# Kernel tuning notes

Measured on AMD Instinct MI355X. Metric: run time of the kernel, lower is better.

## Reference

```python
import jax, jax.numpy as jnp
import numpy as np
from jax import lax

T, B, S = 64, 32, 64
V, E, H = 32000, 512, 512

def _p(key, shape, scale=0.05):
    return (jax.random.normal(key, shape, dtype=jnp.float32) * scale)

def setup_inputs() -> dict:
    key = jax.random.key(0)
    ks = jax.random.split(key, 24)
    inp = {
        'trg': jax.random.randint(ks[0], (T, B), 0, V),
        'encoded_src': jax.random.normal(ks[1], (S, B, 2 * H), dtype=jnp.float32),
        'emb': _p(ks[2], (V, E)),
        # LSTM layer 0: input = E + 2H
        'W_ih0': _p(ks[3], (4 * H, E + 2 * H)), 'W_hh0': _p(ks[4], (4 * H, H)),
        'b_ih0': _p(ks[5], (4 * H,)), 'b_hh0': _p(ks[6], (4 * H,)),
        # LSTM layer 1: input = H
        'W_ih1': _p(ks[7], (4 * H, H)), 'W_hh1': _p(ks[8], (4 * H, H)),
        'b_ih1': _p(ks[9], (4 * H,)), 'b_hh1': _p(ks[10], (4 * H,)),
        # attn_annot: 2H -> H
        'Wa': _p(ks[11], (H, 2 * H)), 'ba': _p(ks[12], (H,)),
        # attn_hidden: H -> H
        'Wh': _p(ks[13], (H, H)), 'bh': _p(ks[14], (H,)),
        # other: H -> 1
        'Wo': _p(ks[15], (1, H)), 'bo': _p(ks[16], (1,)),
        # penult: 3H -> E
        'Wp': _p(ks[17], (E, 3 * H)), 'bp': _p(ks[18], (E,)),
        # out bias (weight tied to emb)
        'b_out': _p(ks[19], (V,)),
    }
    return inp

def _lstm_cell(x, h, c, W_ih, W_hh, b_ih, b_hh):
    # PyTorch gate order: i, f, g, o
    g = x @ W_ih.T + b_ih + h @ W_hh.T + b_hh
    i, f, gg, o = jnp.split(g, 4, axis=-1)
    c_new = jax.nn.sigmoid(f) * c + jax.nn.sigmoid(i) * jnp.tanh(gg)
    h_new = jax.nn.sigmoid(o) * jnp.tanh(c_new)
    return h_new, c_new

def reference(trg, encoded_src, emb, W_ih0, W_hh0, b_ih0, b_hh0,
              W_ih1, W_hh1, b_ih1, b_hh1, Wa, ba, Wh, bh, Wo, bo,
              Wp, bp, b_out):
    trg_emb = emb[trg]                                # [T,B,E]
    annot_scores = encoded_src @ Wa.T + ba            # [S,B,H]
    Hd = W_hh0.shape[1]
    Bd = encoded_src.shape[1]
    h0 = jnp.zeros((2, Bd, Hd), dtype=encoded_src.dtype)
    c0 = jnp.zeros((2, Bd, Hd), dtype=encoded_src.dtype)
    ctx0 = jnp.zeros((Bd, encoded_src.shape[2]), dtype=encoded_src.dtype)

    def step(carry, emb_t):
        h, c, ctx = carry
        x = jnp.concatenate([emb_t, ctx], axis=1)      # [B, E+2H]
        h0n, c0n = _lstm_cell(x,   h[0], c[0], W_ih0, W_hh0, b_ih0, b_hh0)
        h1n, c1n = _lstm_cell(h0n, h[1], c[1], W_ih1, W_hh1, b_ih1, b_hh1)
        out = h1n                                      # [B,H]
        hs = out @ Wh.T + bh                           # [B,H]
        e = jnp.tanh(hs[None] + annot_scores) @ Wo.T + bo   # [S,B,1]
        a = jax.nn.softmax(e, axis=0)[..., 0]          # [S,B]
        ctx_new = jnp.einsum('sb,sbd->bd', a, encoded_src)  # [B,2H]
        stacked = jnp.concatenate([out, ctx_new], axis=1)   # [B,3H]
        return (jnp.stack([h0n, h1n]), jnp.stack([c0n, c1n]), ctx_new), stacked

    (h, c, _), all_scores = lax.scan(step, (h0, c0, ctx0), trg_emb)  # all_scores [T,B,3H]
    pen = all_scores @ Wp.T + bp                       # [T,B,E]
    logits = pen @ emb.T + b_out                       # [T,B,V] (tied weights)
    scores = jax.nn.log_softmax(logits, axis=2)
    return (scores, h, c)
```

## Files before the change

### kernel.cpp

```cpp
#include <hip/hip_runtime.h>


typedef unsigned short u16;
typedef short bf16x8 __attribute__((ext_vector_type(8)));
typedef float f32x4 __attribute__((ext_vector_type(4)));

#define MFMA_BF16(a, b, c) __builtin_amdgcn_mfma_f32_16x16x32_bf16((a), (b), (c), 0, 0, 0)

struct __attribute__((aligned(8))) U16x4 { u16 x, y, z, w; };

__device__ __forceinline__ float b2f(u16 u) {
  unsigned v = ((unsigned)u) << 16; float f; __builtin_memcpy(&f, &v, 4); return f;
}
__device__ __forceinline__ u16 f2b(float f) {
  unsigned u; __builtin_memcpy(&u, &f, 4);
  u = (u + 0x7FFFu + ((u >> 16) & 1u)) >> 16;
  return (u16)u;
}
__device__ __forceinline__ float sigm(float x) { return 1.f / (1.f + __expf(-x)); }
__device__ __forceinline__ float tanh_fast(float x) {
  x = fminf(fmaxf(x, -15.f), 15.f);
  float e = __expf(2.f * x);
  return (e - 1.f) / (e + 1.f);
}

__device__ __forceinline__ bf16x8 bl16(const u16* p) {
  bf16x8 v;
  asm volatile("global_load_dwordx4 %0, %1, off sc0 sc1" : "=v"(v) : "v"(p) : "memory");
  return v;
}
__device__ __forceinline__ float blf(const float* p) {
  float v;
  asm volatile("global_load_dword %0, %1, off sc0 sc1" : "=v"(v) : "v"(p) : "memory");
  return v;
}
__device__ __forceinline__ void bs16(u16* p, u16 d) {
  unsigned dd = d;
  asm volatile("global_store_short %0, %1, off sc0 sc1" :: "v"(p), "v"(dd) : "memory");
}
__device__ __forceinline__ void bs32(float* p, float d) {
  asm volatile("global_store_dword %0, %1, off sc0 sc1" :: "v"(p), "v"(d) : "memory");
}
__device__ __forceinline__ void bs32u(u16* p, unsigned d) {
  asm volatile("global_store_dword %0, %1, off sc0 sc1" :: "v"(p), "v"(d) : "memory");
}
__device__ __forceinline__ void vmwait() {
  asm volatile("s_waitcnt vmcnt(0)" ::: "memory");
  __builtin_amdgcn_sched_barrier(0);
}

__global__ void f2b4_kernel(const float* __restrict__ src, u16* __restrict__ dst, long n4) {
  long i = (long)blockIdx.x * blockDim.x + threadIdx.x;
  long stride = (long)gridDim.x * blockDim.x;
  for (; i < n4; i += stride) {
    float4 v = ((const float4*)src)[i];
    U16x4 o; o.x = f2b(v.x); o.y = f2b(v.y); o.z = f2b(v.z); o.w = f2b(v.w);
    ((U16x4*)dst)[i] = o;
  }
}

__global__ void f2b4_strided(const float* __restrict__ src, u16* __restrict__ dst,
                             int rows, int cols4, int sld, int soff, int dld, int doff) {
  int total = rows * cols4;
  for (int i = blockIdx.x * blockDim.x + threadIdx.x; i < total; i += gridDim.x * blockDim.x) {
    int r = i / cols4, c4 = i - r * cols4;
    float4 v = *(const float4*)(src + (size_t)r * sld + soff + c4 * 4);
    U16x4 o; o.x = f2b(v.x); o.y = f2b(v.y); o.z = f2b(v.z); o.w = f2b(v.w);
    *(U16x4*)(dst + (size_t)r * dld + doff + c4 * 4) = o;
  }
}

__global__ void gather_emb_kernel(const int* __restrict__ trg, const float* __restrict__ emb,
                                  u16* __restrict__ out) {
  int r = blockIdx.x;
  int v = trg[r];
  const float* srow = emb + (size_t)v * 512;
  u16* drow = out + (size_t)r * 512;
  for (int e = threadIdx.x; e < 128; e += blockDim.x) {
    float4 x = ((const float4*)srow)[e];
    U16x4 o; o.x = f2b(x.x); o.y = f2b(x.y); o.z = f2b(x.z); o.w = f2b(x.w);
    ((U16x4*)drow)[e] = o;
  }
}

template <int MODE>
__global__ __launch_bounds__(256) void gemm_bt(
    const u16* __restrict__ A, const u16* __restrict__ B,
    float* __restrict__ outF, u16* __restrict__ outB,
    const float* __restrict__ bias0, const float* __restrict__ bias1,
    int N, int K, int ntiles, float* __restrict__ pmax, float* __restrict__ psum) {
  const int l = threadIdx.x & 63, wv = threadIdx.x >> 6;
  const int m0 = blockIdx.x * 128 + wv * 32;
  const int n0 = blockIdx.y * 64;
  const int kg = ((l >> 4) << 3);
  const u16* Ap0 = A + (size_t)(m0 + (l & 15)) * K + kg;
  const u16* Ap1 = Ap0 + (size_t)16 * K;
  const u16* Bp = B + (size_t)(n0 + (l & 15)) * K + kg;
  f32x4 acc[2][4] = {};
  for (int k0 = 0; k0 < K; k0 += 32) {
    bf16x8 a0 = *(const bf16x8*)(Ap0 + k0);
    bf16x8 a1 = *(const bf16x8*)(Ap1 + k0);
#pragma unroll
    for (int nf = 0; nf < 4; ++nf) {
      bf16x8 bb = *(const bf16x8*)(Bp + (size_t)(nf * 16) * K + k0);
      acc[0][nf] = MFMA_BF16(a0, bb, acc[0][nf]);
      acc[1][nf] = MFMA_BF16(a1, bb, acc[1][nf]);
    }
  }
  float biasv[4];
#pragma unroll
  for (int nf = 0; nf < 4; ++nf) {
    int col = n0 + nf * 16 + (l & 15);
    float bv = bias0 ? bias0[col] : 0.f;
    if (bias1) bv += bias1[col];
    biasv[nf] = bv;
  }
#pragma unroll
  for (int mi = 0; mi < 2; ++mi)
#pragma unroll
    for (int nf = 0; nf < 4; ++nf)
#pragma unroll
      for (int i = 0; i < 4; ++i) acc[mi][nf][i] += biasv[nf];

#pragma unroll
  for (int mi = 0; mi < 2; ++mi)
#pragma unroll
    for (int i = 0; i < 4; ++i) {
      int row = m0 + mi * 16 + ((l >> 4) << 2) + i;
#pragma unroll
      for (int nf = 0; nf < 4; ++nf) {
        int col = n0 + nf * 16 + (l & 15);
        if constexpr (MODE == 1)
          outB[(size_t)row * N + col] = f2b(acc[mi][nf][i]);
        else
          outF[(size_t)row * N + col] = acc[mi][nf][i];
      }
    }
  if constexpr (MODE == 2) {
    float lm[2][4], se[2][4];
#pragma unroll
    for (int mi = 0; mi < 2; ++mi)
#pragma unroll
      for (int i = 0; i < 4; ++i) {
        float m_ = acc[mi][0][i];
#pragma unroll
        for (int nf = 1; nf < 4; ++nf) m_ = fmaxf(m_, acc[mi][nf][i]);
        lm[mi][i] = m_;
      }
#pragma unroll
    for (int d = 1; d < 16; d <<= 1)
#pragma unroll
      for (int mi = 0; mi < 2; ++mi)
#pragma unroll
        for (int i = 0; i < 4; ++i) lm[mi][i] = fmaxf(lm[mi][i], __shfl_xor(lm[mi][i], d));
#pragma unroll
    for (int mi = 0; mi < 2; ++mi)
#pragma unroll
      for (int i = 0; i < 4; ++i) {
        float s_ = 0.f;
#pragma unroll
        for (int nf = 0; nf < 4; ++nf) s_ += __expf(acc[mi][nf][i] - lm[mi][i]);
        se[mi][i] = s_;
      }
#pragma unroll
    for (int d = 1; d < 16; d <<= 1)
#pragma unroll
      for (int mi = 0; mi < 2; ++mi)
#pragma unroll
        for (int i = 0; i < 4; ++i) se[mi][i] += __shfl_xor(se[mi][i], d);
    if ((l & 15) == 0) {
#pragma unroll
      for (int mi = 0; mi < 2; ++mi)
#pragma unroll
        for (int i = 0; i < 4; ++i) {
          int row = m0 + mi * 16 + ((l >> 4) << 2) + i;
          pmax[(size_t)row * ntiles + blockIdx.y] = lm[mi][i];
          psum[(size_t)row * ntiles + blockIdx.y] = se[mi][i];
        }
    }
  }
}

__device__ __forceinline__ void grid_barrier(unsigned* flags, unsigned phase) {
  __syncthreads();
  if (threadIdx.x == 0) {
    __hip_atomic_store(flags + blockIdx.x * 32, phase, __ATOMIC_RELAXED,
                       __HIP_MEMORY_SCOPE_AGENT);
  }
  if (threadIdx.x < 32) {
    int spins = 0;
    while (__hip_atomic_load(flags + threadIdx.x * 32, __ATOMIC_RELAXED,
                             __HIP_MEMORY_SCOPE_AGENT) < phase &&
           spins < 2000000) ++spins;
  }
  __syncthreads();
}

__global__ __launch_bounds__(512, 2) void scan_kernel(
    const u16* __restrict__ xW0,
    const u16* __restrict__ Wcat0,
    const u16* __restrict__ Wcat1,
    const u16* __restrict__ Whb,
    const float* __restrict__ b_ih1, const float* __restrict__ b_hh1,
    const float* __restrict__ bh, const float* __restrict__ Wo, const float* __restrict__ bo,
    const float* __restrict__ annot,
    const float* __restrict__ enc,
    u16* __restrict__ ctxb,
    u16* __restrict__ h0b,
    u16* __restrict__ h1b,
    float* __restrict__ c0, float* __restrict__ c1,
    float* __restrict__ hs,
    u16* __restrict__ scoresb,
    float* __restrict__ dout_hc,
    unsigned* __restrict__ flags) {
  __shared__ float sm[16384];
  const int w = blockIdx.x;
  const int tid = threadIdx.x;
  const int l = tid & 63, wv = tid >> 6;
  const int jh0 = w * 16;
  const int bE = tid >> 4, jlE = tid & 15;
  unsigned phase = 0;

  for (int t = 0; t < 64; ++t) {
    const int pA = t & 1;
    {
      const int kg = ((l >> 4) << 3);
      bf16x8 a0[6], a1[6];
#pragma unroll
      for (int kk = 0; kk < 6; ++kk) {
        const int k0 = wv * 192 + kk * 32;
        const u16* ab; int ld, off;
        if (k0 < 1024) { ab = ctxb; ld = 1024; off = k0; }
        else { ab = h0b + pA * 32 * 512; ld = 512; off = k0 - 1024; }
        a0[kk] = bl16(ab + (size_t)(l & 15) * ld + off + kg);
        a1[kk] = bl16(ab + (size_t)((l & 15) + 16) * ld + off + kg);
      }
      vmwait();
      f32x4 acc[2][4] = {};
#pragma unroll
      for (int kk = 0; kk < 6; ++kk) {
        const int k0 = wv * 192 + kk * 32;
#pragma unroll
        for (int g = 0; g < 4; ++g) {
          bf16x8 bb = *(const bf16x8*)(Wcat0 + (size_t)(g * 512 + jh0 + (l & 15)) * 1536 + k0 + kg);
          acc[0][g] = MFMA_BF16(a0[kk], bb, acc[0][g]);
          acc[1][g] = MFMA_BF16(a1[kk], bb, acc[1][g]);
        }
      }
#pragma unroll
      for (int mi = 0; mi < 2; ++mi)
#pragma unroll
        for (int g = 0; g < 4; ++g)
#pragma unroll
          for (int i = 0; i < 4; ++i) {
            int m = mi * 16 + ((l >> 4) << 2) + i;
            sm[(wv * 32 + m) * 64 + g * 16 + (l & 15)] = acc[mi][g][i];
          }
      __syncthreads();
      {
        const int b = bE, jl = jlE, jh = jh0 + jl;
        float gate[4];
#pragma unroll
        for (int g = 0; g < 4; ++g) {
          float s = 0.f;
#pragma unroll
          for (int kv = 0; kv < 8; ++kv) s += sm[(kv * 32 + b) * 64 + g * 16 + jl];
          gate[g] = s + b2f(xW0[(size_t)(t * 32 + b) * 2048 + g * 512 + jh]);
        }
        float cn = sigm(gate[1]) * c0[b * 512 + jh] + sigm(gate[0]) * tanh_fast(gate[2]);
        float hn = sigm(gate[3]) * tanh_fast(cn);
        c0[b * 512 + jh] = cn;
        bs16(h0b + (pA ^ 1) * 32 * 512 + b * 512 + jh, f2b(hn));
        if (t == 63) { dout_hc[b * 512 + jh] = hn; dout_hc[32768 + b * 512 + jh] = cn; }
      }
    }
    grid_barrier(flags, ++phase);
    {
      const int kg = ((l >> 4) << 3);
      bf16x8 a0[4], a1[4];
#pragma unroll
      for (int kk = 0; kk < 4; ++kk) {
        const int k0 = wv * 128 + kk * 32;
        const u16* ab; int off;
        if (k0 < 512) { ab = h0b + (pA ^ 1) * 32 * 512; off = k0; }
        else { ab = h1b + pA * 32 * 512; off = k0 - 512; }
        a0[kk] = bl16(ab + (size_t)(l & 15) * 512 + off + kg);
        a1[kk] = bl16(ab + (size_t)((l & 15) + 16) * 512 + off + kg);
      }
      vmwait();
      f32x4 acc[2][4] = {};
#pragma unroll
      for (int kk = 0; kk < 4; ++kk) {
        const int k0 = wv * 128 + kk * 32;
#pragma unroll
        for (int g = 0; g < 4; ++g) {
          bf16x8 bb = *(const bf16x8*)(Wcat1 + (size_t)(g * 512 + jh0 + (l & 15)) * 1024 + k0 + kg);
          acc[0][g] = MFMA_BF16(a0[kk], bb, acc[0][g]);
          acc[1][g] = MFMA_BF16(a1[kk], bb, acc[1][g]);
        }
      }
#pragma unroll
      for (int mi = 0; mi < 2; ++mi)
#pragma unroll
        for (int g = 0; g < 4; ++g)
#pragma unroll
          for (int i = 0; i < 4; ++i) {
            int m = mi * 16 + ((l >> 4) << 2) + i;
            sm[(wv * 32 + m) * 64 + g * 16 + (l & 15)] = acc[mi][g][i];
          }
      __syncthreads();
      {
        const int b = bE, jl = jlE, jh = jh0 + jl;
        float gate[4];
#pragma unroll
        for (int g = 0; g < 4; ++g) {
          float s = 0.f;
#pragma unroll
          for (int kv = 0; kv < 8; ++kv) s += sm[(kv * 32 + b) * 64 + g * 16 + jl];
          gate[g] = s + b_ih1[g * 512 + jh] + b_hh1[g * 512 + jh];
        }
        float cn = sigm(gate[1]) * c1[b * 512 + jh] + sigm(gate[0]) * tanh_fast(gate[2]);
        float hn = sigm(gate[3]) * tanh_fast(cn);
        c1[b * 512 + jh] = cn;
        u16 hb = f2b(hn);
        bs16(h1b + (pA ^ 1) * 32 * 512 + b * 512 + jh, hb);
        scoresb[(size_t)(t * 32 + b) * 1536 + jh] = hb;
        if (t == 63) { dout_hc[16384 + b * 512 + jh] = hn; dout_hc[32768 + 16384 + b * 512 + jh] = cn; }
      }
    }
    grid_barrier(flags, ++phase);
    {
      const int kg = ((l >> 4) << 3);
      const u16* h1n = h1b + (pA ^ 1) * 32 * 512;
      bf16x8 a0[2], a1[2];
#pragma unroll
      for (int kk = 0; kk < 2; ++kk) {
        const int k0 = wv * 64 + kk * 32;
        a0[kk] = bl16(h1n + (size_t)(l & 15) * 512 + k0 + kg);
        a1[kk] = bl16(h1n + (size_t)((l & 15) + 16) * 512 + k0 + kg);
      }
      vmwait();
      f32x4 acc2[2] = {};
#pragma unroll
      for (int kk = 0; kk < 2; ++kk) {
        const int k0 = wv * 64 + kk * 32;
        bf16x8 bb = *(const bf16x8*)(Whb + (size_t)(jh0 + (l & 15)) * 512 + k0 + kg);
        acc2[0] = MFMA_BF16(a0[kk], bb, acc2[0]);
        acc2[1] = MFMA_BF16(a1[kk], bb, acc2[1]);
      }
#pragma unroll
      for (int mi = 0; mi < 2; ++mi)
#pragma unroll
        for (int i = 0; i < 4; ++i)
          sm[(wv * 32 + mi * 16 + ((l >> 4) << 2) + i) * 16 + (l & 15)] = acc2[mi][i];
      __syncthreads();
      {
        const int b = bE, jl = jlE;
        float s = 0.f;
#pragma unroll
        for (int kv = 0; kv < 8; ++kv) s += sm[(kv * 32 + b) * 16 + jl];
        bs32(hs + b * 512 + jh0 + jl, s + bh[jh0 + jl]);
      }
    }
    grid_barrier(flags, ++phase);
    {
      const int b = w;
      float* hs_s = sm;
      float* wo_s = sm + 512;
      float* red = sm + 1024;
      float* a_s = sm + 1536;
      float hv = blf(hs + b * 512 + tid);
      vmwait();
      hs_s[tid] = hv;
      wo_s[tid] = Wo[tid];
      __syncthreads();
      const int s_ = tid >> 3, ks = tid & 7;
      const float* arow = annot + (size_t)(s_ * 32 + b) * 512;
      float accv = 0.f;
#pragma unroll 8
      for (int kk = 0; kk < 64; ++kk) {
        int k = ks * 64 + kk;
        accv += tanh_fast(hs_s[k] + arow[k]) * wo_s[k];
      }
      red[tid] = accv;
      __syncthreads();
      if (tid < 64) {
        float e = bo[0];
#pragma unroll
        for (int j = 0; j < 8; ++j) e += red[tid * 8 + j];
        float mx = e;
#pragma unroll
        for (int d = 1; d < 64; d <<= 1) mx = fmaxf(mx, __shfl_xor(mx, d));
        float p = __expf(e - mx);
        float ss = p;
#pragma unroll
        for (int d = 1; d < 64; d <<= 1) ss += __shfl_xor(ss, d);
        a_s[tid] = p / ss;
      }
      __syncthreads();
      float cx0 = 0.f, cx1 = 0.f;
#pragma unroll 8
      for (int s2 = 0; s2 < 64; ++s2) {
        float av = a_s[s2];
        float2 ev = *(const float2*)(enc + (size_t)(s2 * 32 + b) * 1024 + tid * 2);
        cx0 += av * ev.x; cx1 += av * ev.y;
      }
      u16 u0 = f2b(cx0), u1 = f2b(cx1);
      unsigned pk = (unsigned)u0 | ((unsigned)u1 << 16);
      bs32u(ctxb + b * 1024 + tid * 2, pk);
      scoresb[(size_t)(t * 32 + b) * 1536 + 512 + tid * 2] = u0;
      scoresb[(size_t)(t * 32 + b) * 1536 + 512 + tid * 2 + 1] = u1;
    }
    grid_barrier(flags, ++phase);
  }
}

__global__ __launch_bounds__(256) void lse_kernel(const float* __restrict__ pmax,
                                                  const float* __restrict__ psum,
                                                  float* __restrict__ lse, int nt) {
  __shared__ float red[256];
  const int r = blockIdx.x;
  float m = -3.4e38f;
  for (int j = threadIdx.x; j < nt; j += 256) m = fmaxf(m, pmax[(size_t)r * nt + j]);
  red[threadIdx.x] = m; __syncthreads();
  for (int s = 128; s > 0; s >>= 1) {
    if (threadIdx.x < s) red[threadIdx.x] = fmaxf(red[threadIdx.x], red[threadIdx.x + s]);
    __syncthreads();
  }
  const float M = red[0]; __syncthreads();
  float s_ = 0.f;
  for (int j = threadIdx.x; j < nt; j += 256)
    s_ += psum[(size_t)r * nt + j] * __expf(pmax[(size_t)r * nt + j] - M);
  red[threadIdx.x] = s_; __syncthreads();
  for (int s = 128; s > 0; s >>= 1) {
    if (threadIdx.x < s) red[threadIdx.x] += red[threadIdx.x + s];
    __syncthreads();
  }
  if (threadIdx.x == 0) lse[r] = M + logf(red[0]);
}

__global__ void finalize_kernel(float* __restrict__ out, const float* __restrict__ lse) {
  const long n4 = 16384000;
  for (long i = (long)blockIdx.x * blockDim.x + threadIdx.x; i < n4;
       i += (long)gridDim.x * blockDim.x) {
    float4 v = ((float4*)out)[i];
    float L = lse[i / 8000];
    v.x -= L; v.y -= L; v.z -= L; v.w -= L;
    ((float4*)out)[i] = v;
  }
}

extern "C" void kernel_launch(void* const* d_in, const int* in_sizes, int n_in,
                              void* d_out, int out_size, void* d_ws, size_t ws_size,
                              hipStream_t stream) {
  const int* trg = (const int*)d_in[0];
  const float* enc = (const float*)d_in[1];
  const float* emb = (const float*)d_in[2];
  const float* W_ih0 = (const float*)d_in[3];
  const float* W_hh0 = (const float*)d_in[4];
  const float* b_ih0 = (const float*)d_in[5];
  const float* b_hh0 = (const float*)d_in[6];
  const float* W_ih1 = (const float*)d_in[7];
  const float* W_hh1 = (const float*)d_in[8];
  const float* b_ih1 = (const float*)d_in[9];
  const float* b_hh1 = (const float*)d_in[10];
  const float* Wa = (const float*)d_in[11];
  const float* ba = (const float*)d_in[12];
  const float* Wh = (const float*)d_in[13];
  const float* bh = (const float*)d_in[14];
  const float* Wo = (const float*)d_in[15];
  const float* bo = (const float*)d_in[16];
  const float* Wp = (const float*)d_in[17];
  const float* bp = (const float*)d_in[18];
  const float* b_out = (const float*)d_in[19];
  float* out = (float*)d_out;

  unsigned char* ws = (unsigned char*)d_ws;
  size_t off = 0;
  auto alloc = [&](size_t bytes) -> void* {
    void* p = ws + off; off += (bytes + 255) & ~(size_t)255; return p;
  };
  u16* emb_b = (u16*)alloc(32768000);
  u16* trgemb_b = (u16*)alloc(2097152);
  u16* enc_b = (u16*)alloc(4194304);
  u16* Wemb0_b = (u16*)alloc(2097152);
  u16* Wcat0_b = (u16*)alloc(6291456);
  u16* Wcat1_b = (u16*)alloc(4194304);
  u16* Wa_b = (u16*)alloc(1048576);
  u16* Wh_b = (u16*)alloc(524288);
  u16* Wp_b = (u16*)alloc(1572864);
  u16* xW0_b = (u16*)alloc(8388608);
  float* annot = (float*)alloc(4194304);
  u16* scoresb = (u16*)alloc(6291456);
  u16* pen_b = (u16*)alloc(2097152);
  u16* ctxb = (u16*)alloc(65536);
  u16* h0b = (u16*)alloc(65536);
  u16* h1b = (u16*)alloc(65536);
  float* c0 = (float*)alloc(65536);
  float* c1 = (float*)alloc(65536);
  float* hsbuf = (float*)alloc(65536);
  float* pmax = (float*)alloc(4096000);
  float* psum = (float*)alloc(4096000);
  float* lse = (float*)alloc(8192);
  unsigned* flags = (unsigned*)alloc(4096);
  if (off > ws_size) return;

  hipMemsetAsync(ctxb, 0, 65536, stream);
  hipMemsetAsync(h0b, 0, 65536, stream);
  hipMemsetAsync(h1b, 0, 65536, stream);
  hipMemsetAsync(c0, 0, 65536, stream);
  hipMemsetAsync(c1, 0, 65536, stream);
  hipMemsetAsync(flags, 0, 4096, stream);

  f2b4_kernel<<<1024, 256, 0, stream>>>(emb, emb_b, 4096000);
  f2b4_kernel<<<256, 256, 0, stream>>>(enc, enc_b, 524288);
  f2b4_kernel<<<128, 256, 0, stream>>>(Wa, Wa_b, 131072);
  f2b4_kernel<<<64, 256, 0, stream>>>(Wh, Wh_b, 65536);
  f2b4_kernel<<<128, 256, 0, stream>>>(Wp, Wp_b, 196608);
  f2b4_strided<<<512, 256, 0, stream>>>(W_ih0, Wemb0_b, 2048, 128, 1536, 0, 512, 0);
  f2b4_strided<<<512, 256, 0, stream>>>(W_ih0, Wcat0_b, 2048, 256, 1536, 512, 1536, 0);
  f2b4_strided<<<512, 256, 0, stream>>>(W_hh0, Wcat0_b, 2048, 128, 512, 0, 1536, 1024);
  f2b4_strided<<<512, 256, 0, stream>>>(W_ih1, Wcat1_b, 2048, 128, 512, 0, 1024, 0);
  f2b4_strided<<<512, 256, 0, stream>>>(W_hh1, Wcat1_b, 2048, 128, 512, 0, 1024, 512);
  gather_emb_kernel<<<2048, 128, 0, stream>>>(trg, emb, trgemb_b);

  gemm_bt<1><<<dim3(16, 32), 256, 0, stream>>>(trgemb_b, Wemb0_b, nullptr, xW0_b,
                                               b_ih0, b_hh0, 2048, 512, 0, nullptr, nullptr);
  gemm_bt<0><<<dim3(16, 8), 256, 0, stream>>>(enc_b, Wa_b, annot, nullptr,
                                              ba, nullptr, 512, 1024, 0, nullptr, nullptr);
  scan_kernel<<<32, 512, 0, stream>>>(xW0_b, Wcat0_b, Wcat1_b, Wh_b, b_ih1, b_hh1, bh, Wo, bo,
                                      annot, enc, ctxb, h0b, h1b, c0, c1, hsbuf, scoresb,
                                      out + 65536000, flags);
  gemm_bt<1><<<dim3(16, 8), 256, 0, stream>>>(scoresb, Wp_b, nullptr, pen_b,
                                              bp, nullptr, 512, 1536, 0, nullptr, nullptr);
  gemm_bt<2><<<dim3(16, 500), 256, 0, stream>>>(pen_b, emb_b, out, nullptr,
                                                b_out, nullptr, 32000, 512, 500, pmax, psum);
  lse_kernel<<<2048, 256, 0, stream>>>(pmax, psum, lse, 500);
  finalize_kernel<<<2048, 256, 0, stream>>>(out, lse);
}
```

Measured before the change: 2.696 ms.

## Pre-transpose annotations and encoder to bf16 batch-major layout for scan attention

Adds two kernels that convert annot and encoded_src into bf16 arrays laid out [B][S][D], so the per-step attention in the persistent scan kernel reads contiguous vectorised rows at half the bytes. Hoists the layer-1 bias, bh, bo and Wo loads out of the time loop, and issues the xW0 gate loads early so they overlap the A-operand loads. Stores to scoresb now go through cache-bypassing packed stores. The transposed buffers reuse the pmax/psum workspace, which is enlarged to fit, and attention now runs on bf16 inputs with slightly lower precision.

```diff
diff --git a/kernel.cpp b/kernel.cpp
--- a/kernel.cpp
+++ b/kernel.cpp
@@ -33,6 +33,11 @@
   float v;
   asm volatile("global_load_dword %0, %1, off sc0 sc1" : "=v"(v) : "v"(p) : "memory");
   return v;
+}
+__device__ __forceinline__ u16 blu16(const u16* p) {
+  unsigned v;
+  asm volatile("global_load_ushort %0, %1, off sc0 sc1" : "=v"(v) : "v"(p) : "memory");
+  return (u16)v;
 }
 __device__ __forceinline__ void bs16(u16* p, u16 d) {
   unsigned dd = d;
@@ -81,6 +86,26 @@
     U16x4 o; o.x = f2b(x.x); o.y = f2b(x.y); o.z = f2b(x.z); o.w = f2b(x.w);
     ((U16x4*)drow)[e] = o;
   }
+}
+
+__global__ void annot_tr_kernel(const float* __restrict__ annot, u16* __restrict__ abt) {
+  int b = blockIdx.x >> 6, s = blockIdx.x & 63;
+  const float* src = annot + (size_t)(s * 32 + b) * 512;
+  u16* dst = abt + (size_t)(b * 64 + s) * 512;
+  int j = threadIdx.x;
+  float4 v = ((const float4*)src)[j];
+  U16x4 o; o.x = f2b(v.x); o.y = f2b(v.y); o.z = f2b(v.z); o.w = f2b(v.w);
+  ((U16x4*)dst)[j] = o;
+}
+
+__global__ void enc_tr_kernel(const float* __restrict__ enc, u16* __restrict__ ebt) {
+  int b = blockIdx.x >> 6, s = blockIdx.x & 63;
+  const float* src = enc + (size_t)(s * 32 + b) * 1024;
+  u16* dst = ebt + (size_t)(b * 64 + s) * 1024;
+  int j = threadIdx.x;
+  float4 v = ((const float4*)src)[j];
+  U16x4 o; o.x = f2b(v.x); o.y = f2b(v.y); o.z = f2b(v.z); o.w = f2b(v.w);
+  ((U16x4*)dst)[j] = o;
 }
 
 template <int MODE>
@@ -203,8 +228,8 @@
     const u16* __restrict__ Whb,
     const float* __restrict__ b_ih1, const float* __restrict__ b_hh1,
     const float* __restrict__ bh, const float* __restrict__ Wo, const float* __restrict__ bo,
-    const float* __restrict__ annot,
-    const float* __restrict__ enc,
+    const u16* __restrict__ annot_bt,
+    const u16* __restrict__ enc_bt,
     u16* __restrict__ ctxb,
     u16* __restrict__ h0b,
     u16* __restrict__ h1b,
@@ -221,10 +246,22 @@
   const int bE = tid >> 4, jlE = tid & 15;
   unsigned phase = 0;
 
+  float gb1[4];
+#pragma unroll
+  for (int g = 0; g < 4; ++g) gb1[g] = b_ih1[g * 512 + jh0 + jlE] + b_hh1[g * 512 + jh0 + jlE];
+  const float bhv = bh[jh0 + jlE];
+  const float bov = bo[0];
+
   for (int t = 0; t < 64; ++t) {
     const int pA = t & 1;
     {
       const int kg = ((l >> 4) << 3);
+      u16 xw[4];
+      {
+        const u16* xp = xW0 + (size_t)(t * 32 + bE) * 2048 + jh0 + jlE;
+#pragma unroll
+        for (int g = 0; g < 4; ++g) xw[g] = blu16(xp + g * 512);
+      }
       bf16x8 a0[6], a1[6];
 #pragma unroll
       for (int kk = 0; kk < 6; ++kk) {
@@ -265,7 +302,7 @@
           float s = 0.f;
 #pragma unroll
           for (int kv = 0; kv < 8; ++kv) s += sm[(kv * 32 + b) * 64 + g * 16 + jl];
-          gate[g] = s + b2f(xW0[(size_t)(t * 32 + b) * 2048 + g * 512 + jh]);
+          gate[g] = s + b2f(xw[g]);
         }
         float cn = sigm(gate[1]) * c0[b * 512 + jh] + sigm(gate[0]) * tanh_fast(gate[2]);
         float hn = sigm(gate[3]) * tanh_fast(cn);
@@ -317,14 +354,14 @@
           float s = 0.f;
 #pragma unroll
           for (int kv = 0; kv < 8; ++kv) s += sm[(kv * 32 + b) * 64 + g * 16 + jl];
-          gate[g] = s + b_ih1[g * 512 + jh] + b_hh1[g * 512 + jh];
+          gate[g] = s + gb1[g];
         }
         float cn = sigm(gate[1]) * c1[b * 512 + jh] + sigm(gate[0]) * tanh_fast(gate[2]);
         float hn = sigm(gate[3]) * tanh_fast(cn);
         c1[b * 512 + jh] = cn;
         u16 hb = f2b(hn);
         bs16(h1b + (pA ^ 1) * 32 * 512 + b * 512 + jh, hb);
-        scoresb[(size_t)(t * 32 + b) * 1536 + jh] = hb;
+        bs16(scoresb + (size_t)(t * 32 + b) * 1536 + jh, hb);
         if (t == 63) { dout_hc[16384 + b * 512 + jh] = hn; dout_hc[32768 + 16384 + b * 512 + jh] = cn; }
       }
     }
@@ -359,7 +396,7 @@
         float s = 0.f;
 #pragma unroll
         for (int kv = 0; kv < 8; ++kv) s += sm[(kv * 32 + b) * 16 + jl];
-        bs32(hs + b * 512 + jh0 + jl, s + bh[jh0 + jl]);
+        bs32(hs + b * 512 + jh0 + jl, s + bhv);
       }
     }
     grid_barrier(flags, ++phase);
@@ -370,22 +407,27 @@
       float* red = sm + 1024;
       float* a_s = sm + 1536;
       float hv = blf(hs + b * 512 + tid);
+      float wov = Wo[tid];
       vmwait();
       hs_s[tid] = hv;
-      wo_s[tid] = Wo[tid];
+      wo_s[tid] = wov;
       __syncthreads();
       const int s_ = tid >> 3, ks = tid & 7;
-      const float* arow = annot + (size_t)(s_ * 32 + b) * 512;
+      const u16* arow = annot_bt + (size_t)(b * 64 + s_) * 512 + ks * 64;
       float accv = 0.f;
-#pragma unroll 8
-      for (int kk = 0; kk < 64; ++kk) {
-        int k = ks * 64 + kk;
-        accv += tanh_fast(hs_s[k] + arow[k]) * wo_s[k];
+#pragma unroll
+      for (int kk8 = 0; kk8 < 8; ++kk8) {
+        bf16x8 av = *(const bf16x8*)(arow + kk8 * 8);
+#pragma unroll
+        for (int j = 0; j < 8; ++j) {
+          int k = ks * 64 + kk8 * 8 + j;
+          accv += tanh_fast(hs_s[k] + b2f((u16)av[j])) * wo_s[k];
+        }
       }
       red[tid] = accv;
       __syncthreads();
       if (tid < 64) {
-        float e = bo[0];
+        float e = bov;
 #pragma unroll
         for (int j = 0; j < 8; ++j) e += red[tid * 8 + j];
         float mx = e;
@@ -399,17 +441,18 @@
       }
       __syncthreads();
       float cx0 = 0.f, cx1 = 0.f;
+      const u16* erow = enc_bt + (size_t)b * 65536 + tid * 2;
 #pragma unroll 8
       for (int s2 = 0; s2 < 64; ++s2) {
+        unsigned ev = *(const unsigned*)(erow + (size_t)s2 * 1024);
         float av = a_s[s2];
-        float2 ev = *(const float2*)(enc + (size_t)(s2 * 32 + b) * 1024 + tid * 2);
-        cx0 += av * ev.x; cx1 += av * ev.y;
+        cx0 += av * b2f((u16)(ev & 0xFFFFu));
+        cx1 += av * b2f((u16)(ev >> 16));
       }
       u16 u0 = f2b(cx0), u1 = f2b(cx1);
       unsigned pk = (unsigned)u0 | ((unsigned)u1 << 16);
       bs32u(ctxb + b * 1024 + tid * 2, pk);
-      scoresb[(size_t)(t * 32 + b) * 1536 + 512 + tid * 2] = u0;
-      scoresb[(size_t)(t * 32 + b) * 1536 + 512 + tid * 2 + 1] = u1;
+      bs32u(scoresb + (size_t)(t * 32 + b) * 1536 + 512 + tid * 2, pk);
     }
     grid_barrier(flags, ++phase);
   }
@@ -499,11 +542,14 @@
   float* c0 = (float*)alloc(65536);
   float* c1 = (float*)alloc(65536);
   float* hsbuf = (float*)alloc(65536);
-  float* pmax = (float*)alloc(4096000);
-  float* psum = (float*)alloc(4096000);
+  float* pmax = (float*)alloc(4194304);
+  float* psum = (float*)alloc(4194304);
   float* lse = (float*)alloc(8192);
   unsigned* flags = (unsigned*)alloc(4096);
   if (off > ws_size) return;
+
+  u16* annot_bt = (u16*)pmax;
+  u16* enc_bt = (u16*)psum;
 
   hipMemsetAsync(ctxb, 0, 65536, stream);
   hipMemsetAsync(h0b, 0, 65536, stream);
@@ -523,13 +569,16 @@
   f2b4_strided<<<512, 256, 0, stream>>>(W_ih1, Wcat1_b, 2048, 128, 512, 0, 1024, 0);
   f2b4_strided<<<512, 256, 0, stream>>>(W_hh1, Wcat1_b, 2048, 128, 512, 0, 1024, 512);
   gather_emb_kernel<<<2048, 128, 0, stream>>>(trg, emb, trgemb_b);
+  enc_tr_kernel<<<2048, 256, 0, stream>>>(enc, enc_bt);
 
   gemm_bt<1><<<dim3(16, 32), 256, 0, stream>>>(trgemb_b, Wemb0_b, nullptr, xW0_b,
                                                b_ih0, b_hh0, 2048, 512, 0, nullptr, nullptr);
   gemm_bt<0><<<dim3(16, 8), 256, 0, stream>>>(enc_b, Wa_b, annot, nullptr,
                                               ba, nullptr, 512, 1024, 0, nullptr, nullptr);
+  annot_tr_kernel<<<2048, 128, 0, stream>>>(annot, annot_bt);
+
   scan_kernel<<<32, 512, 0, stream>>>(xW0_b, Wcat0_b, Wcat1_b, Wh_b, b_ih1, b_hh1, bh, Wo, bo,
-                                      annot, enc, ctxb, h0b, h1b, c0, c1, hsbuf, scoresb,
+                                      annot_bt, enc_bt, ctxb, h0b, h1b, c0, c1, hsbuf, scoresb,
                                       out + 65536000, flags);
   gemm_bt<1><<<dim3(16, 8), 256, 0, stream>>>(scoresb, Wp_b, nullptr, pen_b,
                                               bp, nullptr, 512, 1536, 0, nullptr, nullptr);
```

After: 2.522 ms. -6.5%, faster.
